# Performance work log

Hardware: AMD Instinct MI355X
Metric: run time of the kernel (lower is better)

The kernel has to match this reference:

```python
import jax, jax.numpy as jnp
import numpy as np

TOP_K_PCT = 0.1
MAX_SHARP_TOKENS = 10
SMOOTHING = 0.1


def setup_inputs() -> dict:
    key = jax.random.key(0)
    logits = jax.random.normal(key, (2, 8, 2048, 2048), dtype=jnp.float32)
    return {"logits": logits, "dim": 3}


def reference(logits, dim):
    # Move the softmax axis to the end so lax.top_k / row-scatter apply.
    x = jnp.moveaxis(logits, dim, -1)
    N = x.shape[-1]
    k = min(MAX_SHARP_TOKENS, max(1, int(N * TOP_K_PCT)))

    vals, idx = jax.lax.top_k(x, k)            # [..., k], sorted descending
    topk_soft = jax.nn.softmax(vals, axis=-1)  # softmax over just the top-k values

    flat = x.reshape(-1, N)                    # [R, N]
    fidx = idx.reshape(-1, k)                  # [R, k]
    rows = jnp.arange(flat.shape[0])[:, None]

    # boolean mask of top-k positions
    mask = jnp.zeros(flat.shape, dtype=bool).at[rows, fidx].set(True)

    # softmax over the remaining (non-top-k) logits; top-k filled with dtype min
    neg_inf = jnp.finfo(flat.dtype).min
    remaining = jnp.where(mask, neg_inf, flat)
    rem_soft = jax.nn.softmax(remaining, axis=-1)
    rem_soft = jnp.where(mask, jnp.zeros((), flat.dtype), rem_soft)

    # scatter top-k softmax back, then blend
    final = jnp.zeros_like(flat).at[rows, fidx].set(topk_soft.reshape(-1, k))
    out = final * (1.0 - SMOOTHING) + rem_soft * SMOOTHING

    return jnp.moveaxis(out.reshape(x.shape), -1, dim)
```

## Files before the change

kernel.cpp:

```cpp
#include <hip/hip_runtime.h>
#include <math.h>

#define ROW_N 2048
#define KSEL 10
#define WCAP 64

typedef float f32x4 __attribute__((ext_vector_type(4)));

__global__ __launch_bounds__(256) void topk_softmax_kernel(
    const float* __restrict__ in, float* __restrict__ out)
{
    const int tid  = threadIdx.x;
    const int lane = tid & 63;
    const int wave = tid >> 6;
    const size_t base = ((size_t)blockIdx.x * 4 + wave) * ROW_N;

    __shared__ unsigned long long s_cand[4][WCAP];

    const f32x4* p4 = reinterpret_cast<const f32x4*>(in + base);
    f32x4 v4[8];
    #pragma unroll
    for (int j = 0; j < 8; ++j) v4[j] = p4[j * 64 + lane];

    float s = 0.f, q = 0.f, vm = -INFINITY;
    #pragma unroll
    for (int j = 0; j < 8; ++j)
        #pragma unroll
        for (int c = 0; c < 4; ++c) {
            float x = v4[j][c];
            s += x; q = fmaf(x, x, q); vm = fmaxf(vm, x);
        }
    #pragma unroll
    for (int off = 32; off > 0; off >>= 1) {
        s += __shfl_xor(s, off);
        q += __shfl_xor(q, off);
        vm = fmaxf(vm, __shfl_xor(vm, off));
    }
    const float mu    = s * (1.f / ROW_N);
    const float sig   = sqrtf(fmaxf(q * (1.f / ROW_N) - mu * mu, 1e-20f));
    const float shift = fmaf(4.f, sig, mu);
    const float vmax  = vm;
    float Tf = fmaf(2.2f, sig, mu);

    float tot = 0.f;
    #pragma unroll
    for (int j = 0; j < 8; ++j)
        #pragma unroll
        for (int c = 0; c < 4; ++c)
            tot += __expf(v4[j][c] - shift);
    #pragma unroll
    for (int off = 32; off > 0; off >>= 1) tot += __shfl_xor(tot, off);

    auto collect = [&](float T) -> int {
        int cnt = 0;
        #pragma unroll
        for (int j = 0; j < 8; ++j)
            #pragma unroll
            for (int c = 0; c < 4; ++c) {
                bool cond = v4[j][c] > T;
                unsigned long long m = __ballot(cond);
                if (cond) {
                    int idx = j * 256 + lane * 4 + c;
                    uint32_t u  = __float_as_uint(v4[j][c]);
                    uint32_t ov = u ^ ((uint32_t)((int32_t)u >> 31) | 0x80000000u);
                    int pos = cnt + (int)__builtin_amdgcn_mbcnt_hi(
                                        (unsigned)(m >> 32),
                                        __builtin_amdgcn_mbcnt_lo((unsigned)m, 0u));
                    if (pos < WCAP)
                        s_cand[wave][pos] = ((unsigned long long)ov << 16) |
                                            (unsigned)(2047 - idx);
                }
                cnt += __popcll(m);
            }
        return cnt;
    };

    int C = collect(Tf);
    int tries = 0;
    while ((C < KSEL || C > WCAP) && tries < 8) {
        Tf += (C < KSEL) ? (-0.5f * sig) : (0.5f * sig);
        C = collect(Tf);
        ++tries;
    }
    if (C > WCAP) C = WCAP;

    unsigned long long k0 = (lane < C) ? s_cand[wave][lane] : 0ULL;

    unsigned long long kmin = 0ULL;
    #pragma unroll
    for (int b = 47; b >= 0; --b) {
        unsigned long long trial = kmin | (1ULL << b);
        unsigned long long m = __ballot(k0 >= trial);
        if (__popcll(m) >= KSEL) kmin = trial;
    }

    uint32_t ovk = (uint32_t)(k0 >> 16);
    float val = __uint_as_float(ovk ^ ((ovk & 0x80000000u) ? 0x80000000u
                                                          : 0xFFFFFFFFu));
    float ee = (k0 >= kmin) ? __expf(val - vmax) : 0.f;
    float ssum = ee;
    #pragma unroll
    for (int off = 32; off > 0; off >>= 1) ssum += __shfl_xor(ssum, off);

    const float tsum = ssum * __expf(vmax - shift);
    const float rem  = tot - tsum;
    const float aa   = 0.9f / ssum;
    const float bb   = 0.1f / rem;

    f32x4* o4 = reinterpret_cast<f32x4*>(out + base);
    #pragma unroll
    for (int j = 0; j < 8; ++j) {
        f32x4 o;
        #pragma unroll
        for (int c = 0; c < 4; ++c) {
            float x = v4[j][c];
            int idx = j * 256 + lane * 4 + c;
            uint32_t u  = __float_as_uint(x);
            uint32_t ov = u ^ ((uint32_t)((int32_t)u >> 31) | 0x80000000u);
            unsigned long long key = ((unsigned long long)ov << 16) |
                                     (unsigned)(2047 - idx);
            bool sel = key >= kmin;
            o[c] = __expf(x - (sel ? vmax : shift)) * (sel ? aa : bb);
        }
        __builtin_nontemporal_store(o, o4 + j * 64 + lane);
    }
}

extern "C" void kernel_launch(void* const* d_in, const int* in_sizes, int n_in,
                              void* d_out, int out_size, void* d_ws, size_t ws_size,
                              hipStream_t stream) {
    const float* logits = (const float*)d_in[0];
    float* out = (float*)d_out;
    const int rows = out_size / ROW_N;
    topk_softmax_kernel<<<dim3(rows / 4), dim3(256), 0, stream>>>(logits, out);
}
```

Baseline: 444.8 us.

## Process four rows per wave with double-buffered register prefetch and scatter top-k

Each wave now handles four rows, loading the next row into a second register buffer while the current one is processed, so global loads overlap with compute. The exp is computed once per element and reused for both the row total and the output, and the top-k outputs are written afterwards as a scatter of ten values instead of being recomputed per element with key comparisons. Holding two 32-float buffers raises register pressure and may lower occupancy. The grid is four times smaller, and the s_waitcnt before the scatter makes the top-k writes wait for the bulk stores.

```diff
diff --git a/kernel.cpp b/kernel.cpp
--- a/kernel.cpp
+++ b/kernel.cpp
@@ -4,125 +4,132 @@
 #define ROW_N 2048
 #define KSEL 10
 #define WCAP 64
+#define RPW  4
 
 typedef float f32x4 __attribute__((ext_vector_type(4)));
+typedef unsigned long long u64;
 
 __global__ __launch_bounds__(256) void topk_softmax_kernel(
-    const float* __restrict__ in, float* __restrict__ out)
+    const float* __restrict__ in, float* __restrict__ out, int nw)
 {
-    const int tid  = threadIdx.x;
-    const int lane = tid & 63;
-    const int wave = tid >> 6;
-    const size_t base = ((size_t)blockIdx.x * 4 + wave) * ROW_N;
+    const int lane = threadIdx.x & 63;
+    const int wave = threadIdx.x >> 6;
+    const int wid  = blockIdx.x * 4 + wave;
 
-    __shared__ unsigned long long s_cand[4][WCAP];
+    __shared__ u64 s_cand[4][WCAP];
 
-    const f32x4* p4 = reinterpret_cast<const f32x4*>(in + base);
-    f32x4 v4[8];
-    #pragma unroll
-    for (int j = 0; j < 8; ++j) v4[j] = p4[j * 64 + lane];
+    f32x4 A[8], B[8];
 
-    float s = 0.f, q = 0.f, vm = -INFINITY;
-    #pragma unroll
-    for (int j = 0; j < 8; ++j)
+    auto loadrow = [&](f32x4 (&V)[8], int row) {
+        const f32x4* p = reinterpret_cast<const f32x4*>(in + (size_t)row * ROW_N);
         #pragma unroll
-        for (int c = 0; c < 4; ++c) {
-            float x = v4[j][c];
-            s += x; q = fmaf(x, x, q); vm = fmaxf(vm, x);
-        }
-    #pragma unroll
-    for (int off = 32; off > 0; off >>= 1) {
-        s += __shfl_xor(s, off);
-        q += __shfl_xor(q, off);
-        vm = fmaxf(vm, __shfl_xor(vm, off));
-    }
-    const float mu    = s * (1.f / ROW_N);
-    const float sig   = sqrtf(fmaxf(q * (1.f / ROW_N) - mu * mu, 1e-20f));
-    const float shift = fmaf(4.f, sig, mu);
-    const float vmax  = vm;
-    float Tf = fmaf(2.2f, sig, mu);
+        for (int j = 0; j < 8; ++j) V[j] = p[j * 64 + lane];
+    };
 
-    float tot = 0.f;
-    #pragma unroll
-    for (int j = 0; j < 8; ++j)
-        #pragma unroll
-        for (int c = 0; c < 4; ++c)
-            tot += __expf(v4[j][c] - shift);
-    #pragma unroll
-    for (int off = 32; off > 0; off >>= 1) tot += __shfl_xor(tot, off);
+    auto process = [&](f32x4 (&V)[8], int row) {
+        const size_t rbase = (size_t)row * ROW_N;
 
-    auto collect = [&](float T) -> int {
-        int cnt = 0;
+        float s = 0.f, q = 0.f, vm = -INFINITY;
         #pragma unroll
         for (int j = 0; j < 8; ++j)
             #pragma unroll
             for (int c = 0; c < 4; ++c) {
-                bool cond = v4[j][c] > T;
-                unsigned long long m = __ballot(cond);
-                if (cond) {
-                    int idx = j * 256 + lane * 4 + c;
-                    uint32_t u  = __float_as_uint(v4[j][c]);
-                    uint32_t ov = u ^ ((uint32_t)((int32_t)u >> 31) | 0x80000000u);
-                    int pos = cnt + (int)__builtin_amdgcn_mbcnt_hi(
-                                        (unsigned)(m >> 32),
-                                        __builtin_amdgcn_mbcnt_lo((unsigned)m, 0u));
-                    if (pos < WCAP)
-                        s_cand[wave][pos] = ((unsigned long long)ov << 16) |
-                                            (unsigned)(2047 - idx);
+                float x = V[j][c];
+                s += x; q = fmaf(x, x, q); vm = fmaxf(vm, x);
+            }
+        #pragma unroll
+        for (int off = 32; off > 0; off >>= 1) {
+            s += __shfl_xor(s, off);
+            q += __shfl_xor(q, off);
+            vm = fmaxf(vm, __shfl_xor(vm, off));
+        }
+        const float mu    = s * (1.f / ROW_N);
+        const float sig   = sqrtf(fmaxf(q * (1.f / ROW_N) - mu * mu, 1e-20f));
+        const float shift = fmaf(4.f, sig, mu);
+        float Tf = fmaf(2.2f, sig, mu);
+
+        int C = 0;
+        #pragma unroll 1
+        for (int t = 0; t < 8; ++t) {
+            C = 0;
+            #pragma unroll
+            for (int j = 0; j < 8; ++j)
+                #pragma unroll
+                for (int c = 0; c < 4; ++c) {
+                    bool cond = V[j][c] > Tf;
+                    u64 m = __ballot(cond);
+                    if (cond) {
+                        int idx = j * 256 + lane * 4 + c;
+                        uint32_t u  = __float_as_uint(V[j][c]);
+                        uint32_t ov = u ^ ((uint32_t)((int32_t)u >> 31) | 0x80000000u);
+                        int pos = C + (int)__builtin_amdgcn_mbcnt_hi(
+                                          (unsigned)(m >> 32),
+                                          __builtin_amdgcn_mbcnt_lo((unsigned)m, 0u));
+                        if (pos < WCAP)
+                            s_cand[wave][pos] = ((u64)ov << 16) |
+                                                (unsigned)(2047 - idx);
+                    }
+                    C += __popcll(m);
                 }
-                cnt += __popcll(m);
-            }
-        return cnt;
+            if (C >= KSEL && C <= WCAP) break;
+            Tf += (C < KSEL) ? (-0.5f * sig) : (0.5f * sig);
+        }
+        if (C > WCAP) C = WCAP;
+
+        u64 k0 = (lane < C) ? s_cand[wave][lane] : 0ULL;
+
+        float tot = 0.f;
+        #pragma unroll
+        for (int j = 0; j < 8; ++j) {
+            f32x4 e;
+            #pragma unroll
+            for (int c = 0; c < 4; ++c) { e[c] = __expf(V[j][c] - shift); tot += e[c]; }
+            V[j] = e;
+        }
+        #pragma unroll
+        for (int off = 32; off > 0; off >>= 1) tot += __shfl_xor(tot, off);
+
+        u64 kmin = 0ULL;
+        #pragma unroll 1
+        for (int b = 47; b >= 0; --b) {
+            u64 trial = kmin | (1ULL << b);
+            u64 mm = __ballot(k0 >= trial);
+            if (__popcll(mm) >= KSEL) kmin = trial;
+        }
+
+        uint32_t ovk = (uint32_t)(k0 >> 16);
+        float val = __uint_as_float(ovk ^ ((ovk & 0x80000000u) ? 0x80000000u
+                                                              : 0xFFFFFFFFu));
+        const bool win = (lane < C) && (k0 >= kmin);
+        float ee = win ? __expf(val - vm) : 0.f;
+        float ssum = ee;
+        #pragma unroll
+        for (int off = 32; off > 0; off >>= 1) ssum += __shfl_xor(ssum, off);
+
+        const float tsum = ssum * __expf(vm - shift);
+        const float aa   = 0.9f / ssum;
+        const float bb   = 0.1f / (tot - tsum);
+
+        f32x4* o4 = reinterpret_cast<f32x4*>(out + rbase);
+        #pragma unroll
+        for (int j = 0; j < 8; ++j) {
+            f32x4 o;
+            #pragma unroll
+            for (int c = 0; c < 4; ++c) o[c] = V[j][c] * bb;
+            __builtin_nontemporal_store(o, o4 + j * 64 + lane);
+        }
+
+        asm volatile("s_waitcnt vmcnt(0)" ::: "memory");
+        if (win) out[rbase + (2047 - (int)(k0 & 0xFFFFull))] = ee * aa;
     };
 
-    int C = collect(Tf);
-    int tries = 0;
-    while ((C < KSEL || C > WCAP) && tries < 8) {
-        Tf += (C < KSEL) ? (-0.5f * sig) : (0.5f * sig);
-        C = collect(Tf);
-        ++tries;
-    }
-    if (C > WCAP) C = WCAP;
-
-    unsigned long long k0 = (lane < C) ? s_cand[wave][lane] : 0ULL;
-
-    unsigned long long kmin = 0ULL;
-    #pragma unroll
-    for (int b = 47; b >= 0; --b) {
-        unsigned long long trial = kmin | (1ULL << b);
-        unsigned long long m = __ballot(k0 >= trial);
-        if (__popcll(m) >= KSEL) kmin = trial;
-    }
-
-    uint32_t ovk = (uint32_t)(k0 >> 16);
-    float val = __uint_as_float(ovk ^ ((ovk & 0x80000000u) ? 0x80000000u
-                                                          : 0xFFFFFFFFu));
-    float ee = (k0 >= kmin) ? __expf(val - vmax) : 0.f;
-    float ssum = ee;
-    #pragma unroll
-    for (int off = 32; off > 0; off >>= 1) ssum += __shfl_xor(ssum, off);
-
-    const float tsum = ssum * __expf(vmax - shift);
-    const float rem  = tot - tsum;
-    const float aa   = 0.9f / ssum;
-    const float bb   = 0.1f / rem;
-
-    f32x4* o4 = reinterpret_cast<f32x4*>(out + base);
-    #pragma unroll
-    for (int j = 0; j < 8; ++j) {
-        f32x4 o;
-        #pragma unroll
-        for (int c = 0; c < 4; ++c) {
-            float x = v4[j][c];
-            int idx = j * 256 + lane * 4 + c;
-            uint32_t u  = __float_as_uint(x);
-            uint32_t ov = u ^ ((uint32_t)((int32_t)u >> 31) | 0x80000000u);
-            unsigned long long key = ((unsigned long long)ov << 16) |
-                                     (unsigned)(2047 - idx);
-            bool sel = key >= kmin;
-            o[c] = __expf(x - (sel ? vmax : shift)) * (sel ? aa : bb);
-        }
-        __builtin_nontemporal_store(o, o4 + j * 64 + lane);
+    loadrow(A, wid);
+    #pragma unroll 1
+    for (int r = 0; r < RPW; r += 2) {
+        loadrow(B, wid + (r + 1) * nw);
+        process(A, wid + r * nw);
+        if (r + 2 < RPW) loadrow(A, wid + (r + 2) * nw);
+        process(B, wid + (r + 1) * nw);
     }
 }
 
@@ -132,5 +139,6 @@
     const float* logits = (const float*)d_in[0];
     float* out = (float*)d_out;
     const int rows = out_size / ROW_N;
-    topk_softmax_kernel<<<dim3(rows / 4), dim3(256), 0, stream>>>(logits, out);
+    const int nw = rows / RPW;
+    topk_softmax_kernel<<<dim3(nw / 4), dim3(256), 0, stream>>>(logits, out, nw);
 }
```

Measured after the change: 472.9 us. 6.3% more time.
